# Optimization experiments

Measured on AMD Instinct MI355X. Metric: run time of the kernel, lower is better.

## Reference

```python
import jax, jax.numpy as jnp
import numpy as np

B, S, D = 4, 2048, 1024


def setup_inputs() -> dict:
    key = jax.random.key(0)
    ks = jax.random.split(key, 4)
    scale = 1.0 / np.sqrt(D)
    x = jax.random.normal(ks[0], (B, S, D), dtype=jnp.float32)
    Wk = jax.random.normal(ks[1], (D, D), dtype=jnp.float32) * scale
    Wq = jax.random.normal(ks[2], (D, D), dtype=jnp.float32) * scale
    Wv = jax.random.normal(ks[3], (D, D), dtype=jnp.float32) * scale
    bk = jnp.zeros((D,), dtype=jnp.float32)
    bq = jnp.zeros((D,), dtype=jnp.float32)
    bv = jnp.zeros((D,), dtype=jnp.float32)
    return {"x": x, "Wk": Wk, "bk": bk, "Wq": Wq, "bq": bq,
            "Wv": Wv, "bv": bv, "dims": 2}


def correlated_weight(k, q, v, dims):
    # correlation between every query position and every key position,
    # scaled by sqrt(d) for numerical stability (standard correlation attn)
    d = q.shape[-1]
    scores = jnp.einsum("bqd,bkd->bqk", q, k) / jnp.sqrt(jnp.asarray(d, q.dtype))
    w = jax.nn.softmax(scores, axis=dims)          # [B, S, S]
    return jnp.einsum("bqk,bkd->bqd", w, v)        # [B, S, D]


def reference(x, Wk, bk, Wq, bq, Wv, bv, dims):
    # injected key/query/value funcs instantiated as Linear layers
    k = jnp.einsum("bsd,de->bse", x, Wk) + bk
    q = jnp.einsum("bsd,de->bse", x, Wq) + bq
    v = jnp.einsum("bsd,de->bse", x, Wv) + bv
    return correlated_weight(k, q, v, dims)
```

## Files before the change

### kernel.cpp

```cpp
#include <hip/hip_runtime.h>
#include <hip/hip_bf16.h>
#include <stdint.h>


typedef unsigned short u16;
typedef __bf16 bf16x8 __attribute__((ext_vector_type(8)));
typedef float  f32x16 __attribute__((ext_vector_type(16)));
typedef u16    u16x4  __attribute__((ext_vector_type(4)));
typedef u16    u16x8  __attribute__((ext_vector_type(8)));

__device__ __forceinline__ u16 f2bf(float f) {
  union { float f; uint32_t u; } v; v.f = f;
  uint32_t r = v.u + 0x7fffu + ((v.u >> 16) & 1u);
  return (u16)(r >> 16);
}
__device__ __forceinline__ float bf2f(u16 b) {
  union { uint32_t u; float f; } v; v.u = (uint32_t)b << 16; return v.f;
}

#define GLD_LDS16(gp, lp) __builtin_amdgcn_global_load_lds(                   \
    (const __attribute__((address_space(1))) void*)(gp),                      \
    (__attribute__((address_space(3))) void*)(lp), 16, 0, 0)


__global__ __launch_bounds__(256) void conv_x(const float* __restrict__ in,
                                              u16* __restrict__ out, int n) {
  int i = (blockIdx.x * 256 + threadIdx.x) * 4;
  if (i >= n) return;
  float4 v = *(const float4*)(in + i);
  u16x4 o; o.x = f2bf(v.x); o.y = f2bf(v.y); o.z = f2bf(v.z); o.w = f2bf(v.w);
  *(u16x4*)(out + i) = o;
}

__global__ __launch_bounds__(256) void trans_conv_w3(const float* __restrict__ Wq,
                                                     const float* __restrict__ Wk,
                                                     const float* __restrict__ Wv,
                                                     u16* __restrict__ Wt) {
  __shared__ float t[32][33];
  const float* W = blockIdx.z == 0 ? Wq : (blockIdx.z == 1 ? Wk : Wv);
  u16* dst = Wt + (size_t)blockIdx.z * 1024 * 1024;
  int e0 = blockIdx.x * 32, d0 = blockIdx.y * 32;
  #pragma unroll
  for (int i = 0; i < 4; ++i)
    t[threadIdx.y + i * 8][threadIdx.x] =
        W[(size_t)(d0 + threadIdx.y + i * 8) * 1024 + e0 + threadIdx.x];
  __syncthreads();
  #pragma unroll
  for (int i = 0; i < 4; ++i)
    dst[(size_t)(e0 + threadIdx.y + i * 8) * 1024 + d0 + threadIdx.x] =
        f2bf(t[threadIdx.x][threadIdx.y + i * 8]);
}

__global__ __launch_bounds__(256) void concat_bias(const float* __restrict__ bq,
                                                   const float* __restrict__ bk,
                                                   const float* __restrict__ bv,
                                                   float* __restrict__ bc) {
  int i = blockIdx.x * 256 + threadIdx.x;
  if (i >= 3072) return;
  bc[i] = (i < 1024) ? bq[i] : (i < 2048 ? bk[i - 1024] : bv[i - 2048]);
}

__global__ __launch_bounds__(256) void trans_v(const u16* __restrict__ qkv,
                                               u16* __restrict__ vT) {
  __shared__ u16 t[64][72];
  int b = blockIdx.z;
  int s0 = blockIdx.x * 64, e0 = blockIdx.y * 64;
  const u16* src = qkv + (size_t)b * 2048 * 3072 + 2048;
  u16* dst = vT + (size_t)b * 1024 * 2048;
  int tx = threadIdx.x & 7, ty = threadIdx.x >> 3;
  #pragma unroll
  for (int rr = 0; rr < 64; rr += 32)
    *(u16x8*)&t[ty + rr][tx * 8] =
        *(const u16x8*)(src + (size_t)(s0 + ty + rr) * 3072 + e0 + tx * 8);
  __syncthreads();
  #pragma unroll
  for (int rr = 0; rr < 64; rr += 32) {
    int er = ty + rr;
    u16x8 o;
    #pragma unroll
    for (int j = 0; j < 8; ++j) o[j] = t[tx * 8 + j][er];
    *(u16x8*)(dst + (size_t)(e0 + er) * 2048 + s0 + tx * 8) = o;
  }
}


template <bool OUT_BF16, bool BIAS>
__global__ __launch_bounds__(256)
void gemm_bt(const u16* __restrict__ A, int lda, long long sA,
             const u16* __restrict__ B, int ldb, long long sB,
             void* __restrict__ C, int ldc, long long sC,
             const float* __restrict__ bias, int K, float scale) {
  __shared__ u16 As[128 * 64];
  __shared__ u16 Bs[128 * 64];
  const int lane = threadIdx.x & 63;
  const int wv = threadIdx.x >> 6;

  const u16* Ab = A + (size_t)blockIdx.z * sA + (size_t)blockIdx.y * 128 * lda;
  const u16* Bb = B + (size_t)blockIdx.z * sB + (size_t)blockIdx.x * 128 * ldb;

  const int srow = lane >> 3;
  const int scol = ((lane & 7) ^ (lane >> 3)) * 8;
  const int r32 = lane & 31;
  const int half = lane >> 5;
  const int rx = lane & 7;
  const int wm = (wv >> 1) * 64;
  const int wn = (wv & 1) * 64;

  f32x16 acc[2][2];
  #pragma unroll
  for (int i = 0; i < 2; ++i)
    #pragma unroll
    for (int j = 0; j < 2; ++j) acc[i][j] = (f32x16)0.0f;

  for (int k0 = 0; k0 < K; k0 += 64) {
    #pragma unroll
    for (int i = 0; i < 4; ++i) {
      int r = wv * 32 + i * 8;
      GLD_LDS16(Ab + (size_t)(r + srow) * lda + k0 + scol, As + r * 64);
      GLD_LDS16(Bb + (size_t)(r + srow) * ldb + k0 + scol, Bs + r * 64);
    }
    __syncthreads();

    bf16x8 af[2][4], bfr[2][4];
    #pragma unroll
    for (int i = 0; i < 2; ++i)
      #pragma unroll
      for (int t = 0; t < 4; ++t) {
        int pc = ((t * 2 + half) ^ rx) * 8;
        af[i][t]  = *(const bf16x8*)(As + (wm + i * 32 + r32) * 64 + pc);
        bfr[i][t] = *(const bf16x8*)(Bs + (wn + i * 32 + r32) * 64 + pc);
      }
    #pragma unroll
    for (int i = 0; i < 2; ++i)
      #pragma unroll
      for (int j = 0; j < 2; ++j)
        #pragma unroll
        for (int t = 0; t < 4; ++t)
          acc[i][j] = __builtin_amdgcn_mfma_f32_32x32x16_bf16(
              af[i][t], bfr[j][t], acc[i][j], 0, 0, 0);
    __syncthreads();
  }

  const int ccol0 = blockIdx.x * 128 + wn + r32;
  const int crow0 = blockIdx.y * 128 + wm + 4 * half;
  u16* Cb = (u16*)C + (size_t)blockIdx.z * sC;
  float* Cf = (float*)C + (size_t)blockIdx.z * sC;
  #pragma unroll
  for (int i = 0; i < 2; ++i) {
    #pragma unroll
    for (int e = 0; e < 16; ++e) {
      int m = crow0 + i * 32 + (e & 3) + 8 * (e >> 2);
      #pragma unroll
      for (int j = 0; j < 2; ++j) {
        int n = ccol0 + j * 32;
        float v = acc[i][j][e] * scale;
        if (BIAS) v += bias[n];
        if (OUT_BF16) Cb[(size_t)m * ldc + n] = f2bf(v);
        else          Cf[(size_t)m * ldc + n] = v;
      }
    }
  }
}

__global__ __launch_bounds__(512)
void gemm_bt8(const u16* __restrict__ A, int lda, long long sA,
              const u16* __restrict__ B, int ldb, long long sB,
              float* __restrict__ C, int ldc, long long sC,
              int K, float scale) {
  __shared__ u16 As[128 * 64];
  __shared__ u16 Bs[128 * 64];
  const int lane = threadIdx.x & 63;
  const int wv = threadIdx.x >> 6;

  const u16* Ab = A + (size_t)blockIdx.z * sA + (size_t)blockIdx.y * 128 * lda;
  const u16* Bb = B + (size_t)blockIdx.z * sB + (size_t)blockIdx.x * 128 * ldb;

  const int srow = lane >> 3;
  const int scol = ((lane & 7) ^ (lane >> 3)) * 8;
  const int r32 = lane & 31;
  const int half = lane >> 5;
  const int rx = lane & 7;
  const int wm = (wv >> 2) * 64;
  const int wn = (wv & 3) * 32;

  f32x16 acc[2];
  acc[0] = (f32x16)0.0f; acc[1] = (f32x16)0.0f;

  for (int k0 = 0; k0 < K; k0 += 64) {
    #pragma unroll
    for (int i = 0; i < 2; ++i) {
      int r = wv * 16 + i * 8;
      GLD_LDS16(Ab + (size_t)(r + srow) * lda + k0 + scol, As + r * 64);
      GLD_LDS16(Bb + (size_t)(r + srow) * ldb + k0 + scol, Bs + r * 64);
    }
    __syncthreads();

    bf16x8 af[2][4], bfr[4];
    #pragma unroll
    for (int t = 0; t < 4; ++t) {
      int pc = ((t * 2 + half) ^ rx) * 8;
      af[0][t] = *(const bf16x8*)(As + (wm + r32) * 64 + pc);
      af[1][t] = *(const bf16x8*)(As + (wm + 32 + r32) * 64 + pc);
      bfr[t]   = *(const bf16x8*)(Bs + (wn + r32) * 64 + pc);
    }
    #pragma unroll
    for (int i = 0; i < 2; ++i)
      #pragma unroll
      for (int t = 0; t < 4; ++t)
        acc[i] = __builtin_amdgcn_mfma_f32_32x32x16_bf16(
            af[i][t], bfr[t], acc[i], 0, 0, 0);
    __syncthreads();
  }

  const int ccol = blockIdx.x * 128 + wn + r32;
  const int crow0 = blockIdx.y * 128 + wm + 4 * half;
  float* Cf = C + (size_t)blockIdx.z * sC;
  #pragma unroll
  for (int i = 0; i < 2; ++i)
    #pragma unroll
    for (int e = 0; e < 16; ++e) {
      int m = crow0 + i * 32 + (e & 3) + 8 * (e >> 2);
      Cf[(size_t)m * ldc + ccol] = acc[i][e] * scale;
    }
}


__global__ __launch_bounds__(256) void softmax_rows(u16* __restrict__ P) {
  __shared__ float red[4];
  const int t = threadIdx.x;
  const int lane = t & 63, wv = t >> 6;
  u16* row = P + (size_t)blockIdx.x * 2048;
  u16x8 w = ((const u16x8*)row)[t];
  float v[8];
  #pragma unroll
  for (int j = 0; j < 8; ++j) v[j] = bf2f(w[j]);
  float m = v[0];
  #pragma unroll
  for (int j = 1; j < 8; ++j) m = fmaxf(m, v[j]);
  #pragma unroll
  for (int off = 32; off > 0; off >>= 1) m = fmaxf(m, __shfl_down(m, off));
  if (lane == 0) red[wv] = m;
  __syncthreads();
  m = fmaxf(fmaxf(red[0], red[1]), fmaxf(red[2], red[3]));
  __syncthreads();
  float e[8], s = 0.f;
  #pragma unroll
  for (int j = 0; j < 8; ++j) { e[j] = exp2f((v[j] - m) * 1.44269504f); s += e[j]; }
  #pragma unroll
  for (int off = 32; off > 0; off >>= 1) s += __shfl_down(s, off);
  if (lane == 0) red[wv] = s;
  __syncthreads();
  s = red[0] + red[1] + red[2] + red[3];
  float inv = 1.0f / s;
  u16x8 o;
  #pragma unroll
  for (int j = 0; j < 8; ++j) o[j] = f2bf(e[j] * inv);
  ((u16x8*)row)[t] = o;
}


extern "C" void kernel_launch(void* const* d_in, const int* in_sizes, int n_in,
                              void* d_out, int out_size, void* d_ws, size_t ws_size,
                              hipStream_t stream) {
  const float* x  = (const float*)d_in[0];
  const float* Wk = (const float*)d_in[1];
  const float* bk = (const float*)d_in[2];
  const float* Wq = (const float*)d_in[3];
  const float* bq = (const float*)d_in[4];
  const float* Wv = (const float*)d_in[5];
  const float* bv = (const float*)d_in[6];
  float* out = (float*)d_out;

  char* ws = (char*)d_ws;
  u16*   xb  = (u16*)(ws + 0);
  u16*   wt  = (u16*)(ws + 16777216);
  float* bc  = (float*)(ws + 23068672);
  u16*   qkv = (u16*)(ws + 23080960);
  u16*   vT  = (u16*)(ws + 73412608);
  u16*   P   = (u16*)(ws + 90189824);
  (void)in_sizes; (void)n_in; (void)out_size; (void)ws_size;

  conv_x<<<8192, 256, 0, stream>>>(x, xb, 8388608);
  trans_conv_w3<<<dim3(32, 32, 3), dim3(32, 8), 0, stream>>>(Wq, Wk, Wv, wt);
  concat_bias<<<12, 256, 0, stream>>>(bq, bk, bv, bc);

  gemm_bt<true, true><<<dim3(24, 64, 1), 256, 0, stream>>>(
      xb, 1024, 0LL, wt, 1024, 0LL, (void*)qkv, 3072, 0LL, bc, 1024, 1.0f);

  trans_v<<<dim3(32, 16, 4), 256, 0, stream>>>(qkv, vT);

  gemm_bt<true, false><<<dim3(16, 16, 4), 256, 0, stream>>>(
      qkv, 3072, 2048LL * 3072, qkv + 1024, 3072, 2048LL * 3072,
      (void*)P, 2048, 2048LL * 2048, nullptr, 1024, 0.03125f);

  softmax_rows<<<8192, 256, 0, stream>>>(P);

  gemm_bt8<<<dim3(8, 16, 4), 512, 0, stream>>>(
      P, 2048, 2048LL * 2048, vT, 2048, 1024LL * 2048,
      out, 1024, 2048LL * 1024, 2048, 1.0f);
}
```

Before: 273.8 us.

## Replace 128x128 GEMM with double-buffered 256x256 8-wave pipelined kernel

Replaces the simple 128x128-tile GEMM used for the QKV projection and the QK^T score computation with a 256x256-tile, 512-thread kernel. It double-buffers LDS stages and interleaves global-to-LDS loads with 16x16x32 MFMA quadrants, using s_setprio and explicit waitcnt. It also swizzles the workgroup order for L2 locality. The aim is to hide memory latency and raise data reuse per block. The cost is more LDS (64KB) and fewer blocks, which lowers occupancy and leaves a tail, for example 384 blocks for the QKV GEMM.

```diff
diff --git a/kernel.cpp b/kernel.cpp
--- a/kernel.cpp
+++ b/kernel.cpp
@@ -5,6 +5,7 @@
 
 typedef unsigned short u16;
 typedef __bf16 bf16x8 __attribute__((ext_vector_type(8)));
+typedef float  f32x4  __attribute__((ext_vector_type(4)));
 typedef float  f32x16 __attribute__((ext_vector_type(16)));
 typedef u16    u16x4  __attribute__((ext_vector_type(4)));
 typedef u16    u16x8  __attribute__((ext_vector_type(8)));
@@ -84,77 +85,168 @@
 }
 
 
-template <bool OUT_BF16, bool BIAS>
-__global__ __launch_bounds__(256)
-void gemm_bt(const u16* __restrict__ A, int lda, long long sA,
-             const u16* __restrict__ B, int ldb, long long sB,
-             void* __restrict__ C, int ldc, long long sC,
-             const float* __restrict__ bias, int K, float scale) {
-  __shared__ u16 As[128 * 64];
-  __shared__ u16 Bs[128 * 64];
+#define FENCE8 asm volatile("" ::: "memory")
+#define BARR8  do { FENCE8; __builtin_amdgcn_s_barrier(); FENCE8; } while (0)
+#define WAITL8 asm volatile("s_waitcnt lgkmcnt(0)" ::: "memory")
+#define VMW(N) asm volatile("s_waitcnt vmcnt(" #N ")" ::: "memory")
+
+#define STAGE_A8(S, H, TT) do {                                               \
+    GLD_LDS16(pA[H][0] + (TT) * 64,                                           \
+              As + (S) * 16384 + ((H) * 64 + wv * 8) * 64);                   \
+    GLD_LDS16(pA[H][1] + (TT) * 64,                                           \
+              As + (S) * 16384 + ((H) * 64 + 128 + wv * 8) * 64);             \
+  } while (0)
+
+#define STAGE_B8(S, H, TT) do {                                               \
+    GLD_LDS16(pB[H][0] + (TT) * 64,                                           \
+              Bs + (S) * 16384 + ((H) * 32 + (wv >> 2) * 64 + (wv & 3) * 8) * 64); \
+    GLD_LDS16(pB[H][1] + (TT) * 64,                                           \
+              Bs + (S) * 16384 + ((H) * 32 + 128 + (wv >> 2) * 64 + (wv & 3) * 8) * 64); \
+  } while (0)
+
+#define RD_A8(S, MH) do {                                                     \
+    _Pragma("unroll")                                                         \
+    for (int mf = 0; mf < 4; ++mf) {                                          \
+      const u16* p_ = As + (S) * 16384 + rdA + ((MH) * 64 + mf * 16) * 64;    \
+      a[mf][0] = *(const bf16x8*)(p_ + pos0);                                 \
+      a[mf][1] = *(const bf16x8*)(p_ + pos1);                                 \
+    }                                                                         \
+  } while (0)
+
+#define RD_B8(S, NH) do {                                                     \
+    _Pragma("unroll")                                                         \
+    for (int nf = 0; nf < 2; ++nf) {                                          \
+      const u16* p_ = Bs + (S) * 16384 + rdB + ((NH) * 32 + nf * 16) * 64;    \
+      b[nf][0] = *(const bf16x8*)(p_ + pos0);                                 \
+      b[nf][1] = *(const bf16x8*)(p_ + pos1);                                 \
+    }                                                                         \
+  } while (0)
+
+#define MFMA_Q8(MH, NH) do {                                                  \
+    _Pragma("unroll")                                                         \
+    for (int ks = 0; ks < 2; ++ks)                                            \
+      _Pragma("unroll")                                                       \
+      for (int mf = 0; mf < 4; ++mf)                                          \
+        _Pragma("unroll")                                                     \
+        for (int nf = 0; nf < 2; ++nf)                                        \
+          acc[(MH) * 4 + mf][(NH) * 2 + nf] =                                 \
+              __builtin_amdgcn_mfma_f32_16x16x32_bf16(                        \
+                  a[mf][ks], b[nf][ks], acc[(MH) * 4 + mf][(NH) * 2 + nf],    \
+                  0, 0, 0);                                                   \
+  } while (0)
+
+#define GROUP8(S, T, EN1, EN2, WAITST) do {                                   \
+    RD_A8(S, 0); RD_B8(S, 0);                                                 \
+    if (EN1) STAGE_B8((S) ^ 1, 0, (T) + 1);                                   \
+    BARR8; WAITL8;                                                            \
+    __builtin_amdgcn_s_setprio(1); MFMA_Q8(0, 0);                             \
+    __builtin_amdgcn_s_setprio(0); BARR8;                                     \
+    RD_B8(S, 1);                                                              \
+    if (EN2) STAGE_A8(S, 0, (T) + 2);                                         \
+    BARR8; WAITL8;                                                            \
+    __builtin_amdgcn_s_setprio(1); MFMA_Q8(0, 1);                             \
+    __builtin_amdgcn_s_setprio(0); BARR8;                                     \
+    RD_A8(S, 1);                                                              \
+    if (EN2) STAGE_B8(S, 1, (T) + 2);                                         \
+    BARR8; WAITL8;                                                            \
+    __builtin_amdgcn_s_setprio(1); MFMA_Q8(1, 1);                             \
+    __builtin_amdgcn_s_setprio(0); BARR8;                                     \
+    RD_B8(S, 0);                                                              \
+    if (EN2) STAGE_A8(S, 1, (T) + 2);                                         \
+    BARR8; WAITL8;                                                            \
+    __builtin_amdgcn_s_setprio(1); MFMA_Q8(1, 0);                             \
+    __builtin_amdgcn_s_setprio(0); WAITST; BARR8;                             \
+  } while (0)
+
+template <int NT, bool OUT_BF16, bool BIAS>
+__global__ __launch_bounds__(512)
+void gemm8p(const u16* __restrict__ A, int lda, long long sA,
+            const u16* __restrict__ B, int ldb, long long sB,
+            void* __restrict__ C, int ldc, long long sC,
+            const float* __restrict__ bias, float scale) {
+  __shared__ __align__(16) u16 As[2 * 256 * 64];
+  __shared__ __align__(16) u16 Bs[2 * 256 * 64];
+
   const int lane = threadIdx.x & 63;
-  const int wv = threadIdx.x >> 6;
-
-  const u16* Ab = A + (size_t)blockIdx.z * sA + (size_t)blockIdx.y * 128 * lda;
-  const u16* Bb = B + (size_t)blockIdx.z * sB + (size_t)blockIdx.x * 128 * ldb;
-
+  const int wv   = threadIdx.x >> 6;
+  const int wm   = wv >> 2;
+  const int wn   = wv & 3;
+  const int l15  = lane & 15;
+  const int hi4  = lane >> 4;
+  const int rx7  = lane & 7;
   const int srow = lane >> 3;
-  const int scol = ((lane & 7) ^ (lane >> 3)) * 8;
-  const int r32 = lane & 31;
-  const int half = lane >> 5;
-  const int rx = lane & 7;
-  const int wm = (wv >> 1) * 64;
-  const int wn = (wv & 1) * 64;
-
-  f32x16 acc[2][2];
-  #pragma unroll
-  for (int i = 0; i < 2; ++i)
-    #pragma unroll
-    for (int j = 0; j < 2; ++j) acc[i][j] = (f32x16)0.0f;
-
-  for (int k0 = 0; k0 < K; k0 += 64) {
-    #pragma unroll
-    for (int i = 0; i < 4; ++i) {
-      int r = wv * 32 + i * 8;
-      GLD_LDS16(Ab + (size_t)(r + srow) * lda + k0 + scol, As + r * 64);
-      GLD_LDS16(Bb + (size_t)(r + srow) * ldb + k0 + scol, Bs + r * 64);
-    }
-    __syncthreads();
-
-    bf16x8 af[2][4], bfr[2][4];
-    #pragma unroll
-    for (int i = 0; i < 2; ++i)
-      #pragma unroll
-      for (int t = 0; t < 4; ++t) {
-        int pc = ((t * 2 + half) ^ rx) * 8;
-        af[i][t]  = *(const bf16x8*)(As + (wm + i * 32 + r32) * 64 + pc);
-        bfr[i][t] = *(const bf16x8*)(Bs + (wn + i * 32 + r32) * 64 + pc);
-      }
-    #pragma unroll
-    for (int i = 0; i < 2; ++i)
-      #pragma unroll
-      for (int j = 0; j < 2; ++j)
-        #pragma unroll
-        for (int t = 0; t < 4; ++t)
-          acc[i][j] = __builtin_amdgcn_mfma_f32_32x32x16_bf16(
-              af[i][t], bfr[j][t], acc[i][j], 0, 0, 0);
-    __syncthreads();
-  }
-
-  const int ccol0 = blockIdx.x * 128 + wn + r32;
-  const int crow0 = blockIdx.y * 128 + wm + 4 * half;
+  const int scem = ((lane & 7) ^ srow) * 8;
+
+  const int nx = gridDim.x;
+  const int flat = blockIdx.y * nx + blockIdx.x;
+  const int nwg = nx * gridDim.y;
+  const int cpx = nwg >> 3;
+  const int swz = (flat & 7) * cpx + (flat >> 3);
+  const int bx = swz % nx, by = swz / nx;
+
+  const u16* Ab = A + (size_t)blockIdx.z * sA + (size_t)by * 256 * lda;
+  const u16* Bb = B + (size_t)blockIdx.z * sB + (size_t)bx * 256 * ldb;
+
+  const u16* pA[2][2];
+  const u16* pB[2][2];
+  #pragma unroll
+  for (int h = 0; h < 2; ++h)
+    #pragma unroll
+    for (int r = 0; r < 2; ++r) {
+      pA[h][r] = Ab + (size_t)(h * 64 + r * 128 + wv * 8 + srow) * lda + scem;
+      pB[h][r] = Bb + (size_t)(h * 32 + r * 128 + (wv >> 2) * 64 +
+                               (wv & 3) * 8 + srow) * ldb + scem;
+    }
+
+  const int rdA = (wm * 128 + l15) * 64;
+  const int rdB = (wn * 64 + l15) * 64;
+  const int pos0 = (hi4 ^ rx7) * 8;
+  const int pos1 = ((4 + hi4) ^ rx7) * 8;
+
+  f32x4 acc[8][4];
+  #pragma unroll
+  for (int i = 0; i < 8; ++i)
+    #pragma unroll
+    for (int j = 0; j < 4; ++j) acc[i][j] = (f32x4)0.0f;
+
+  bf16x8 a[4][2], b[2][2];
+
+  STAGE_A8(0, 0, 0); STAGE_B8(0, 1, 0); STAGE_A8(0, 1, 0); STAGE_B8(0, 0, 0);
+  VMW(4);
+  STAGE_A8(1, 0, 1); STAGE_B8(1, 1, 1); STAGE_A8(1, 1, 1);
+  VMW(6);
+  BARR8;
+
+  #pragma unroll 1
+  for (int i = 0; i < NT / 2 - 1; ++i) {
+    const int t0 = 2 * i;
+    GROUP8(0, t0,     1, 1, VMW(6));
+    GROUP8(1, t0 + 1, 1, 1, VMW(6));
+  }
+  GROUP8(0, NT - 2, 1, 0, VMW(0));
+  GROUP8(1, NT - 1, 0, 0, (void)0);
+
+  const int m0 = by * 256 + wm * 128;
+  const int n0 = bx * 256 + wn * 64;
   u16* Cb = (u16*)C + (size_t)blockIdx.z * sC;
   float* Cf = (float*)C + (size_t)blockIdx.z * sC;
-  #pragma unroll
-  for (int i = 0; i < 2; ++i) {
-    #pragma unroll
-    for (int e = 0; e < 16; ++e) {
-      int m = crow0 + i * 32 + (e & 3) + 8 * (e >> 2);
+  float bb[4];
+  if (BIAS) {
+    #pragma unroll
+    for (int fn = 0; fn < 4; ++fn)
+      bb[fn] = bias[n0 + (fn >> 1) * 32 + (fn & 1) * 16 + l15];
+  }
+  #pragma unroll
+  for (int fm = 0; fm < 8; ++fm) {
+    const int mb = m0 + (fm >> 2) * 64 + (fm & 3) * 16 + hi4 * 4;
+    #pragma unroll
+    for (int e = 0; e < 4; ++e) {
+      const int m = mb + e;
       #pragma unroll
-      for (int j = 0; j < 2; ++j) {
-        int n = ccol0 + j * 32;
-        float v = acc[i][j][e] * scale;
-        if (BIAS) v += bias[n];
+      for (int fn = 0; fn < 4; ++fn) {
+        const int n = n0 + (fn >> 1) * 32 + (fn & 1) * 16 + l15;
+        float v = acc[fm][fn][e] * scale;
+        if (BIAS) v += bb[fn];
         if (OUT_BF16) Cb[(size_t)m * ldc + n] = f2bf(v);
         else          Cf[(size_t)m * ldc + n] = v;
       }
@@ -284,14 +376,14 @@
   trans_conv_w3<<<dim3(32, 32, 3), dim3(32, 8), 0, stream>>>(Wq, Wk, Wv, wt);
   concat_bias<<<12, 256, 0, stream>>>(bq, bk, bv, bc);
 
-  gemm_bt<true, true><<<dim3(24, 64, 1), 256, 0, stream>>>(
-      xb, 1024, 0LL, wt, 1024, 0LL, (void*)qkv, 3072, 0LL, bc, 1024, 1.0f);
+  gemm8p<16, true, true><<<dim3(12, 32, 1), 512, 0, stream>>>(
+      xb, 1024, 0LL, wt, 1024, 0LL, (void*)qkv, 3072, 0LL, bc, 1.0f);
 
   trans_v<<<dim3(32, 16, 4), 256, 0, stream>>>(qkv, vT);
 
-  gemm_bt<true, false><<<dim3(16, 16, 4), 256, 0, stream>>>(
+  gemm8p<16, true, false><<<dim3(8, 8, 4), 512, 0, stream>>>(
       qkv, 3072, 2048LL * 3072, qkv + 1024, 3072, 2048LL * 3072,
-      (void*)P, 2048, 2048LL * 2048, nullptr, 1024, 0.03125f);
+      (void*)P, 2048, 2048LL * 2048, nullptr, 0.03125f);
 
   softmax_rows<<<8192, 256, 0, stream>>>(P);
 
```

Measured after the change: 273.8 us. No clear change (+0.0%).
